# Kernel optimization log

Measured on AMD Instinct MI355X. Metric: run time of the kernel, lower is better.

Reference implementation:

```python
import jax, jax.numpy as jnp
import numpy as np

NUM_HEADS = 12
WIN = 7  # window_size[0] == window_size[1]


def setup_inputs() -> dict:
    key = jax.random.key(0)
    ks = jax.random.split(key, 8)
    B_, N, C = 2048, WIN * WIN, 384
    nW = 64
    return {
        "x": jax.random.normal(ks[0], (B_, N, C), dtype=jnp.float32),
        "mask": jax.random.normal(ks[1], (nW, N, N), dtype=jnp.float32),
        "qkv_w": jax.random.normal(ks[2], (3 * C, C), dtype=jnp.float32) * 0.02,
        "qkv_b": jax.random.normal(ks[3], (3 * C,), dtype=jnp.float32) * 0.02,
        "proj_w": jax.random.normal(ks[4], (C, C), dtype=jnp.float32) * 0.02,
        "proj_b": jax.random.normal(ks[5], (C,), dtype=jnp.float32) * 0.02,
        "rpb_table": jax.random.normal(ks[6], ((2 * WIN - 1) ** 2, NUM_HEADS), dtype=jnp.float32) * 0.02,
        "rel_index": jax.random.randint(ks[7], (N * N,), 0, (2 * WIN - 1) ** 2, dtype=jnp.int32),
    }


def reference(x, mask, qkv_w, qkv_b, proj_w, proj_b, rpb_table, rel_index):
    B_, N, C = x.shape
    H = NUM_HEADS
    d = C // H
    scale = d ** -0.5

    # QKV projection (quant wrappers act as identity in non-quant state)
    qkv = x @ qkv_w.T + qkv_b                      # [B_, N, 3C]
    qkv = qkv.reshape(B_, N, 3, H, d).transpose(2, 0, 3, 1, 4)  # [3, B_, H, N, d]
    q, k, v = qkv[0], qkv[1], qkv[2]

    attn = jnp.einsum("bhnd,bhmd->bhnm", q * scale, k)  # [B_, H, N, N]

    # relative position bias gather: [N*N] -> [N, N, H] -> [H, N, N]
    bias = rpb_table[rel_index].reshape(N, N, H).transpose(2, 0, 1)
    attn = attn + bias[None]

    # shifted-window mask add
    nW = mask.shape[0]
    attn = attn.reshape(B_ // nW, nW, H, N, N) + mask[None, :, None]
    attn = attn.reshape(B_, H, N, N)

    attn = jax.nn.softmax(attn, axis=-1)

    out = jnp.einsum("bhnm,bhmd->bhnd", attn, v)   # [B_, H, N, d]
    out = out.transpose(0, 2, 1, 3).reshape(B_, N, C)
    out = out @ proj_w.T + proj_b
    return out, attn
```

## Files before the change

kernel.cpp:

```cpp
#include <hip/hip_runtime.h>
#include <hip/hip_bf16.h>
#include <stdint.h>

#define H_ 12
#define D_ 32
#define N_ 49
#define C_ 384
#define B_TOT 2048
#define BH 24576
#define M_ROWS 100352
#define SCALE 0.17677669529663689f

typedef float f32x4 __attribute__((ext_vector_type(4)));
typedef __bf16 bf16x8 __attribute__((ext_vector_type(8)));
typedef unsigned short ushortx8 __attribute__((ext_vector_type(8)));

static __device__ __forceinline__ unsigned short f2bf(float f) {
  __bf16 b = (__bf16)f;
  return __builtin_bit_cast(unsigned short, b);
}

#define GL16(gp, lp)                                                        \
  __builtin_amdgcn_global_load_lds(                                         \
      (const __attribute__((address_space(1))) unsigned int*)(gp),          \
      (__attribute__((address_space(3))) unsigned int*)(lp), 16, 0, 0)

__global__ void prep(const float* __restrict__ x, const float* __restrict__ wq,
                     const float* __restrict__ wpw, const float* __restrict__ mask,
                     const float* __restrict__ rpb, const int* __restrict__ ridx,
                     unsigned short* __restrict__ x_bf,
                     unsigned short* __restrict__ wq_bf,
                     unsigned short* __restrict__ wp_bf,
                     float* __restrict__ comb) {
  const int blk = blockIdx.x, tid = threadIdx.x;
  if (blk < 2048) {
    for (int i = blk * 256 + tid; i < 4816896; i += 2048 * 256) {
      float4 a = ((const float4*)x)[2 * i];
      float4 b = ((const float4*)x)[2 * i + 1];
      ushortx8 v;
      v[0] = f2bf(a.x); v[1] = f2bf(a.y); v[2] = f2bf(a.z); v[3] = f2bf(a.w);
      v[4] = f2bf(b.x); v[5] = f2bf(b.y); v[6] = f2bf(b.z); v[7] = f2bf(b.w);
      *(ushortx8*)&x_bf[(size_t)i * 8] = v;
    }
  } else if (blk < 2264) {
    const int i = (blk - 2048) * 256 + tid;
    float4 a = ((const float4*)wq)[2 * i];
    float4 b = ((const float4*)wq)[2 * i + 1];
    ushortx8 v;
    v[0] = f2bf(a.x); v[1] = f2bf(a.y); v[2] = f2bf(a.z); v[3] = f2bf(a.w);
    v[4] = f2bf(b.x); v[5] = f2bf(b.y); v[6] = f2bf(b.z); v[7] = f2bf(b.w);
    *(ushortx8*)&wq_bf[(size_t)i * 8] = v;
  } else if (blk < 2336) {
    const int i = (blk - 2264) * 256 + tid;
    float4 a = ((const float4*)wpw)[2 * i];
    float4 b = ((const float4*)wpw)[2 * i + 1];
    ushortx8 v;
    v[0] = f2bf(a.x); v[1] = f2bf(a.y); v[2] = f2bf(a.z); v[3] = f2bf(a.w);
    v[4] = f2bf(b.x); v[5] = f2bf(b.y); v[6] = f2bf(b.z); v[7] = f2bf(b.w);
    *(ushortx8*)&wp_bf[(size_t)i * 8] = v;
  } else {
    const int wh = blk - 2336;
    const int w = wh / 12, h = wh - w * 12;
    float* cb = comb + (size_t)wh * 4096;
    const float* mw = mask + (size_t)w * N_ * N_;
    for (int e = tid; e < 4096; e += 256) {
      const int r = e >> 6, c = e & 63;
      float v;
      if (c >= N_) v = -1e30f;
      else if (r >= N_) v = 0.0f;
      else v = mw[r * N_ + c] + rpb[ridx[r * N_ + c] * H_ + h];
      cb[e] = v;
    }
  }
}

__global__ __launch_bounds__(256, 4)
void qkv_gemm(const unsigned short* __restrict__ A,
              const unsigned short* __restrict__ W,
              const float* __restrict__ bias, unsigned short* __restrict__ qkv) {
  __shared__ __align__(16) unsigned short smem[16384];
  const int tid = threadIdx.x;
  const int w = blockIdx.x;
  const int t = (w & 7) * 882 + (w >> 3);
  const int bm = t / 9, bn = t - bm * 9;
  const int lane = tid & 63, wv = tid >> 6;
  const int wm = wv >> 1, wn = wv & 1;
  const int lo = lane & 15, hi = lane >> 4;

  const int sr0 = tid >> 2, sq0 = (tid & 3) ^ ((sr0 >> 1) & 3);
  const int ci1 = tid + 256;
  const int sr1 = ci1 >> 2, sq1 = (ci1 & 3) ^ ((sr1 >> 1) & 3);

  const unsigned short* Ab = A + (size_t)bm * 128 * 384;
  const unsigned short* Wb = W + (size_t)bn * 128 * 384;

  f32x4 acc[4][4];
#pragma unroll
  for (int i = 0; i < 4; i++)
#pragma unroll
    for (int j = 0; j < 4; j++)
#pragma unroll
      for (int r = 0; r < 4; r++) acc[i][j][r] = 0.0f;

  {
    unsigned short* b0 = smem;
    GL16(Ab + sr0 * 384 + sq0 * 8, b0 + tid * 8);
    GL16(Ab + sr1 * 384 + sq1 * 8, b0 + ci1 * 8);
    GL16(Wb + sr0 * 384 + sq0 * 8, b0 + 4096 + tid * 8);
    GL16(Wb + sr1 * 384 + sq1 * 8, b0 + 4096 + ci1 * 8);
  }
  __syncthreads();

  int buf = 0;
  for (int kt = 0; kt < 12; kt++) {
    if (kt < 11) {
      const int kk = (kt + 1) * 32;
      unsigned short* nb = smem + (buf ^ 1) * 8192;
      GL16(Ab + sr0 * 384 + kk + sq0 * 8, nb + tid * 8);
      GL16(Ab + sr1 * 384 + kk + sq1 * 8, nb + ci1 * 8);
      GL16(Wb + sr0 * 384 + kk + sq0 * 8, nb + 4096 + tid * 8);
      GL16(Wb + sr1 * 384 + kk + sq1 * 8, nb + 4096 + ci1 * 8);
    }
    const unsigned short* ba = smem + buf * 8192;
    bf16x8 af[4], bfm[4];
#pragma unroll
    for (int mt = 0; mt < 4; mt++) {
      const int row = wm * 64 + mt * 16 + lo;
      af[mt] = *(const bf16x8*)&ba[(row * 4 + (hi ^ ((row >> 1) & 3))) * 8];
    }
#pragma unroll
    for (int nt = 0; nt < 4; nt++) {
      const int row = wn * 64 + nt * 16 + lo;
      bfm[nt] = *(const bf16x8*)&ba[4096 + (row * 4 + (hi ^ ((row >> 1) & 3))) * 8];
    }
#pragma unroll
    for (int mt = 0; mt < 4; mt++)
#pragma unroll
      for (int nt = 0; nt < 4; nt++)
        acc[mt][nt] = __builtin_amdgcn_mfma_f32_16x16x32_bf16(af[mt], bfm[nt], acc[mt][nt], 0, 0, 0);
    __syncthreads();
    buf ^= 1;
  }

  unsigned short* ep = smem + wv * 4096;
#pragma unroll
  for (int nt = 0; nt < 4; nt++) {
    const int j = bn * 128 + wn * 64 + nt * 16 + lo;
    const float bj = bias[j];
    const float mul = (j < 384) ? SCALE : 1.0f;
    const int c16 = nt * 2 + (lo >> 3);
    const int wi = lo & 7;
#pragma unroll
    for (int mt = 0; mt < 4; mt++) {
#pragma unroll
      for (int r = 0; r < 4; r++) {
        const int row = mt * 16 + hi * 4 + r;
        ep[row * 64 + ((c16 ^ hi) << 3) + wi] = f2bf((acc[mt][nt][r] + bj) * mul);
      }
    }
  }
#pragma unroll
  for (int cc = 0; cc < 2; cc++) {
    const int cidx = cc * 64 + lane;
    const int lr = cidx >> 1, lch = cidx & 1;
    const int i = bm * 128 + wm * 64 + lr;
    const int b = i / 49, sq = i - b * 49;
    const int j0 = bn * 128 + wn * 64 + lch * 32;
    const int which = j0 / 384;
    const int rem = j0 - which * 384;
    const int h = rem >> 5;
    const int hlr = (lr >> 2) & 3;
    unsigned short* dst = qkv + ((size_t)which * BH + (size_t)b * H_ + h) * (N_ * D_) + sq * D_;
#pragma unroll
    for (int q = 0; q < 4; q++) {
      const int c16r = lch * 4 + q;
      *(uint4*)(dst + q * 8) = *(const uint4*)&ep[lr * 64 + ((c16r ^ hlr) << 3)];
    }
  }
}

__global__ __launch_bounds__(64, 2)
void attn_kernel(const unsigned short* __restrict__ qkv,
                 const float* __restrict__ comb,
                 float* __restrict__ probs,
                 unsigned short* __restrict__ av) {
  __shared__ __align__(16) unsigned short P[64 * 72];
  __shared__ __align__(16) unsigned short VT[32 * 72];
  const int lane = threadIdx.x;
  const int lo = lane & 15, hi = lane >> 4;
  const int h = blockIdx.x, b = blockIdx.y;

  const unsigned short* qp = qkv + (size_t)(b * H_ + h) * (N_ * D_);
  const unsigned short* kp = qp + (size_t)BH * (N_ * D_);
  const unsigned short* vp = kp + (size_t)BH * (N_ * D_);

  {
    unsigned int* vz = (unsigned int*)VT;
#pragma unroll
    for (int i = 0; i < 18; i++) vz[lane + 64 * i] = 0u;
  }
  __syncthreads();

  bf16x8 aq[4], bk[4];
#pragma unroll
  for (int t = 0; t < 4; t++) {
    aq[t] = *(const bf16x8*)(qp + (t * 16 + lo) * D_ + hi * 8);
    bk[t] = *(const bf16x8*)(kp + (t * 16 + lo) * D_ + hi * 8);
  }
  f32x4 s[4][4];
#pragma unroll
  for (int mt = 0; mt < 4; mt++)
#pragma unroll
    for (int nt = 0; nt < 4; nt++) {
#pragma unroll
      for (int r = 0; r < 4; r++) s[mt][nt][r] = 0.0f;
      s[mt][nt] = __builtin_amdgcn_mfma_f32_16x16x32_bf16(aq[mt], bk[nt], s[mt][nt], 0, 0, 0);
    }

#pragma unroll
  for (int it = 0; it < 4; it++) {
    const int idx = it * 64 + lane;
    if (idx < 196) {
      const int sq = idx >> 2, ch = idx & 3;
      ushortx8 vv = *(const ushortx8*)(vp + sq * D_ + ch * 8);
#pragma unroll
      for (int jj = 0; jj < 8; jj++) VT[(ch * 8 + jj) * 72 + sq] = vv[jj];
    }
  }

  const float* cb = comb + (size_t)((b & 63) * H_ + h) * 4096;
#pragma unroll
  for (int mt = 0; mt < 4; mt++) {
#pragma unroll
    for (int r = 0; r < 4; r++) {
      const int row = mt * 16 + hi * 4 + r;
      const float* crow = cb + row * 64 + lo;
      float v0 = s[mt][0][r] + crow[0];
      float v1 = s[mt][1][r] + crow[16];
      float v2 = s[mt][2][r] + crow[32];
      float v3 = s[mt][3][r] + crow[48];
      float m = fmaxf(fmaxf(v0, v1), fmaxf(v2, v3));
      m = fmaxf(m, __shfl_xor(m, 1));
      m = fmaxf(m, __shfl_xor(m, 2));
      m = fmaxf(m, __shfl_xor(m, 4));
      m = fmaxf(m, __shfl_xor(m, 8));
      v0 = __expf(v0 - m); v1 = __expf(v1 - m);
      v2 = __expf(v2 - m); v3 = __expf(v3 - m);
      float sum = v0 + v1 + v2 + v3;
      sum += __shfl_xor(sum, 1);
      sum += __shfl_xor(sum, 2);
      sum += __shfl_xor(sum, 4);
      sum += __shfl_xor(sum, 8);
      const float rinv = 1.0f / sum;
      s[mt][0][r] = v0 * rinv; s[mt][1][r] = v1 * rinv;
      s[mt][2][r] = v2 * rinv; s[mt][3][r] = v3 * rinv;
    }
  }

  const size_t pbase = (size_t)(b * H_ + h) * N_ * N_;
#pragma unroll
  for (int mt = 0; mt < 4; mt++) {
#pragma unroll
    for (int r = 0; r < 4; r++) {
      const int row = mt * 16 + hi * 4 + r;
      if (row < N_) {
#pragma unroll
        for (int nt = 0; nt < 4; nt++) {
          const int c = nt * 16 + lo;
          if (c < N_) probs[pbase + row * N_ + c] = s[mt][nt][r];
        }
      }
#pragma unroll
      for (int nt = 0; nt < 4; nt++)
        P[row * 72 + nt * 16 + lo] = f2bf(s[mt][nt][r]);
    }
  }
  __syncthreads();

  f32x4 o[4][2];
#pragma unroll
  for (int mt = 0; mt < 4; mt++)
#pragma unroll
    for (int n2 = 0; n2 < 2; n2++)
#pragma unroll
      for (int r = 0; r < 4; r++) o[mt][n2][r] = 0.0f;
#pragma unroll
  for (int ks = 0; ks < 2; ks++) {
    bf16x8 pa[4], vb[2];
#pragma unroll
    for (int mt = 0; mt < 4; mt++)
      pa[mt] = *(const bf16x8*)&P[(mt * 16 + lo) * 72 + ks * 32 + hi * 8];
#pragma unroll
    for (int n2 = 0; n2 < 2; n2++)
      vb[n2] = *(const bf16x8*)&VT[(n2 * 16 + lo) * 72 + ks * 32 + hi * 8];
#pragma unroll
    for (int mt = 0; mt < 4; mt++)
#pragma unroll
      for (int n2 = 0; n2 < 2; n2++)
        o[mt][n2] = __builtin_amdgcn_mfma_f32_16x16x32_bf16(pa[mt], vb[n2], o[mt][n2], 0, 0, 0);
  }

  __syncthreads();
#pragma unroll
  for (int mt = 0; mt < 4; mt++) {
#pragma unroll
    for (int r = 0; r < 4; r++) {
      const int row = mt * 16 + hi * 4 + r;
      if (row < N_) {
#pragma unroll
        for (int n2 = 0; n2 < 2; n2++)
          P[row * 40 + n2 * 16 + lo] = f2bf(o[mt][n2][r]);
      }
    }
  }
  if (lane < N_) {
    unsigned short* dst = av + ((size_t)b * N_ + lane) * C_ + h * D_;
    const unsigned short* src = P + lane * 40;
#pragma unroll
    for (int q = 0; q < 4; q++)
      *(uint4*)(dst + q * 8) = *(const uint4*)(src + q * 8);
  }
}

__global__ __launch_bounds__(256, 4)
void proj_gemm(const unsigned short* __restrict__ A,
               const unsigned short* __restrict__ W,
               const float* __restrict__ bias, float* __restrict__ out) {
  __shared__ __align__(16) unsigned short smem[16384];
  const int tid = threadIdx.x;
  const int w = blockIdx.x;
  const int t = (w & 7) * 294 + (w >> 3);
  const int bm = t / 3, bn = t - bm * 3;
  const int lane = tid & 63, wv = tid >> 6;
  const int wm = wv >> 1, wn = wv & 1;
  const int lo = lane & 15, hi = lane >> 4;

  const int sr0 = tid >> 2, sq0 = (tid & 3) ^ ((sr0 >> 1) & 3);
  const int ci1 = tid + 256;
  const int sr1 = ci1 >> 2, sq1 = (ci1 & 3) ^ ((sr1 >> 1) & 3);

  const unsigned short* Ab = A + (size_t)bm * 128 * 384;
  const unsigned short* Wb = W + (size_t)bn * 128 * 384;

  f32x4 acc[4][4];
#pragma unroll
  for (int i = 0; i < 4; i++)
#pragma unroll
    for (int j = 0; j < 4; j++)
#pragma unroll
      for (int r = 0; r < 4; r++) acc[i][j][r] = 0.0f;

  {
    unsigned short* b0 = smem;
    GL16(Ab + sr0 * 384 + sq0 * 8, b0 + tid * 8);
    GL16(Ab + sr1 * 384 + sq1 * 8, b0 + ci1 * 8);
    GL16(Wb + sr0 * 384 + sq0 * 8, b0 + 4096 + tid * 8);
    GL16(Wb + sr1 * 384 + sq1 * 8, b0 + 4096 + ci1 * 8);
  }
  __syncthreads();

  int buf = 0;
  for (int kt = 0; kt < 12; kt++) {
    if (kt < 11) {
      const int kk = (kt + 1) * 32;
      unsigned short* nb = smem + (buf ^ 1) * 8192;
      GL16(Ab + sr0 * 384 + kk + sq0 * 8, nb + tid * 8);
      GL16(Ab + sr1 * 384 + kk + sq1 * 8, nb + ci1 * 8);
      GL16(Wb + sr0 * 384 + kk + sq0 * 8, nb + 4096 + tid * 8);
      GL16(Wb + sr1 * 384 + kk + sq1 * 8, nb + 4096 + ci1 * 8);
    }
    const unsigned short* ba = smem + buf * 8192;
    bf16x8 af[4], bfm[4];
#pragma unroll
    for (int mt = 0; mt < 4; mt++) {
      const int row = wm * 64 + mt * 16 + lo;
      af[mt] = *(const bf16x8*)&ba[(row * 4 + (hi ^ ((row >> 1) & 3))) * 8];
    }
#pragma unroll
    for (int nt = 0; nt < 4; nt++) {
      const int row = wn * 64 + nt * 16 + lo;
      bfm[nt] = *(const bf16x8*)&ba[4096 + (row * 4 + (hi ^ ((row >> 1) & 3))) * 8];
    }
#pragma unroll
    for (int mt = 0; mt < 4; mt++)
#pragma unroll
      for (int nt = 0; nt < 4; nt++)
        acc[mt][nt] = __builtin_amdgcn_mfma_f32_16x16x32_bf16(af[mt], bfm[nt], acc[mt][nt], 0, 0, 0);
    __syncthreads();
    buf ^= 1;
  }

#pragma unroll
  for (int nt = 0; nt < 4; nt++) {
    const int j = bn * 128 + wn * 64 + nt * 16 + lo;
    const float bj = bias[j];
#pragma unroll
    for (int mt = 0; mt < 4; mt++) {
#pragma unroll
      for (int r = 0; r < 4; r++) {
        const int i = bm * 128 + wm * 64 + mt * 16 + hi * 4 + r;
        out[(size_t)i * 384 + j] = acc[mt][nt][r] + bj;
      }
    }
  }
}

extern "C" void kernel_launch(void* const* d_in, const int* in_sizes, int n_in,
                              void* d_out, int out_size, void* d_ws, size_t ws_size,
                              hipStream_t stream) {
  const float* x      = (const float*)d_in[0];
  const float* mask   = (const float*)d_in[1];
  const float* qkv_w  = (const float*)d_in[2];
  const float* qkv_b  = (const float*)d_in[3];
  const float* proj_w = (const float*)d_in[4];
  const float* proj_b = (const float*)d_in[5];
  const float* rpb    = (const float*)d_in[6];
  const int*   ridx   = (const int*)d_in[7];

  unsigned short* qkv   = (unsigned short*)d_ws;
  unsigned short* x_bf  = qkv + (size_t)3 * BH * N_ * D_;
  unsigned short* av    = x_bf;
  float* comb           = (float*)(x_bf + (size_t)M_ROWS * C_);
  unsigned short* wq_bf = (unsigned short*)(comb + 768 * 4096);
  unsigned short* wp_bf = wq_bf + 1152 * 384;
  float* out   = (float*)d_out;
  float* probs = out + (size_t)M_ROWS * C_;

  prep<<<3104, 256, 0, stream>>>(x, qkv_w, proj_w, mask, rpb, ridx,
                                 x_bf, wq_bf, wp_bf, comb);
  qkv_gemm<<<7056, 256, 0, stream>>>(x_bf, wq_bf, qkv_b, qkv);
  attn_kernel<<<dim3(H_, B_TOT), 64, 0, stream>>>(qkv, comb, probs, av);
  proj_gemm<<<2352, 256, 0, stream>>>(av, wp_bf, proj_b, out);
}
```

Before: 459.4 us.

## Fuse fp32-to-bf16 conversion of x into QKV GEMM loads and swizzle attention LDS

The QKV GEMM now reads fp32 activations directly through registers, converts them to bf16 and writes them into swizzled shared memory, so the separate conversion pass over x and its bf16 buffer disappear from prep. Each A tile is now read 9 times in fp32 across the N-blocks instead of in bf16, which doubles A-side global traffic in the GEMM, and occupancy is lowered to 3 blocks per CU to make room for the extra registers. Separately, the attention kernel's P and V^T shared buffers drop their padding in favour of an XOR swizzle to avoid bank conflicts.

```diff
diff --git a/kernel.cpp b/kernel.cpp
--- a/kernel.cpp
+++ b/kernel.cpp
@@ -20,46 +20,37 @@
   return __builtin_bit_cast(unsigned short, b);
 }
 
+static __device__ __forceinline__ uint4 pack8(float4 a, float4 b) {
+  ushortx8 v;
+  v[0] = f2bf(a.x); v[1] = f2bf(a.y); v[2] = f2bf(a.z); v[3] = f2bf(a.w);
+  v[4] = f2bf(b.x); v[5] = f2bf(b.y); v[6] = f2bf(b.z); v[7] = f2bf(b.w);
+  return __builtin_bit_cast(uint4, v);
+}
+
 #define GL16(gp, lp)                                                        \
   __builtin_amdgcn_global_load_lds(                                         \
       (const __attribute__((address_space(1))) unsigned int*)(gp),          \
       (__attribute__((address_space(3))) unsigned int*)(lp), 16, 0, 0)
 
-__global__ void prep(const float* __restrict__ x, const float* __restrict__ wq,
-                     const float* __restrict__ wpw, const float* __restrict__ mask,
-                     const float* __restrict__ rpb, const int* __restrict__ ridx,
-                     unsigned short* __restrict__ x_bf,
+__global__ void prep(const float* __restrict__ wq, const float* __restrict__ wpw,
+                     const float* __restrict__ mask, const float* __restrict__ rpb,
+                     const int* __restrict__ ridx,
                      unsigned short* __restrict__ wq_bf,
                      unsigned short* __restrict__ wp_bf,
                      float* __restrict__ comb) {
   const int blk = blockIdx.x, tid = threadIdx.x;
-  if (blk < 2048) {
-    for (int i = blk * 256 + tid; i < 4816896; i += 2048 * 256) {
-      float4 a = ((const float4*)x)[2 * i];
-      float4 b = ((const float4*)x)[2 * i + 1];
-      ushortx8 v;
-      v[0] = f2bf(a.x); v[1] = f2bf(a.y); v[2] = f2bf(a.z); v[3] = f2bf(a.w);
-      v[4] = f2bf(b.x); v[5] = f2bf(b.y); v[6] = f2bf(b.z); v[7] = f2bf(b.w);
-      *(ushortx8*)&x_bf[(size_t)i * 8] = v;
-    }
-  } else if (blk < 2264) {
-    const int i = (blk - 2048) * 256 + tid;
+  if (blk < 216) {
+    const int i = blk * 256 + tid;
     float4 a = ((const float4*)wq)[2 * i];
     float4 b = ((const float4*)wq)[2 * i + 1];
-    ushortx8 v;
-    v[0] = f2bf(a.x); v[1] = f2bf(a.y); v[2] = f2bf(a.z); v[3] = f2bf(a.w);
-    v[4] = f2bf(b.x); v[5] = f2bf(b.y); v[6] = f2bf(b.z); v[7] = f2bf(b.w);
-    *(ushortx8*)&wq_bf[(size_t)i * 8] = v;
-  } else if (blk < 2336) {
-    const int i = (blk - 2264) * 256 + tid;
+    *(uint4*)&wq_bf[(size_t)i * 8] = pack8(a, b);
+  } else if (blk < 288) {
+    const int i = (blk - 216) * 256 + tid;
     float4 a = ((const float4*)wpw)[2 * i];
     float4 b = ((const float4*)wpw)[2 * i + 1];
-    ushortx8 v;
-    v[0] = f2bf(a.x); v[1] = f2bf(a.y); v[2] = f2bf(a.z); v[3] = f2bf(a.w);
-    v[4] = f2bf(b.x); v[5] = f2bf(b.y); v[6] = f2bf(b.z); v[7] = f2bf(b.w);
-    *(ushortx8*)&wp_bf[(size_t)i * 8] = v;
+    *(uint4*)&wp_bf[(size_t)i * 8] = pack8(a, b);
   } else {
-    const int wh = blk - 2336;
+    const int wh = blk - 288;
     const int w = wh / 12, h = wh - w * 12;
     float* cb = comb + (size_t)wh * 4096;
     const float* mw = mask + (size_t)w * N_ * N_;
@@ -74,8 +65,8 @@
   }
 }
 
-__global__ __launch_bounds__(256, 4)
-void qkv_gemm(const unsigned short* __restrict__ A,
+__global__ __launch_bounds__(256, 3)
+void qkv_gemm(const float* __restrict__ A,
               const unsigned short* __restrict__ W,
               const float* __restrict__ bias, unsigned short* __restrict__ qkv) {
   __shared__ __align__(16) unsigned short smem[16384];
@@ -87,11 +78,14 @@
   const int wm = wv >> 1, wn = wv & 1;
   const int lo = lane & 15, hi = lane >> 4;
 
+  const int arow = tid >> 1, acg = tid & 1;
+  const int ac0 = (acg * 2) ^ ((arow >> 1) & 3);
+  const int ac1 = (acg * 2 + 1) ^ ((arow >> 1) & 3);
   const int sr0 = tid >> 2, sq0 = (tid & 3) ^ ((sr0 >> 1) & 3);
   const int ci1 = tid + 256;
   const int sr1 = ci1 >> 2, sq1 = (ci1 & 3) ^ ((sr1 >> 1) & 3);
 
-  const unsigned short* Ab = A + (size_t)bm * 128 * 384;
+  const float* Ab = A + (size_t)bm * 128 * 384 + arow * 384 + acg * 16;
   const unsigned short* Wb = W + (size_t)bn * 128 * 384;
 
   f32x4 acc[4][4];
@@ -103,21 +97,27 @@
       for (int r = 0; r < 4; r++) acc[i][j][r] = 0.0f;
 
   {
-    unsigned short* b0 = smem;
-    GL16(Ab + sr0 * 384 + sq0 * 8, b0 + tid * 8);
-    GL16(Ab + sr1 * 384 + sq1 * 8, b0 + ci1 * 8);
-    GL16(Wb + sr0 * 384 + sq0 * 8, b0 + 4096 + tid * 8);
-    GL16(Wb + sr1 * 384 + sq1 * 8, b0 + 4096 + ci1 * 8);
+    float4 s0 = *(const float4*)(Ab + 0);
+    float4 s1 = *(const float4*)(Ab + 4);
+    float4 s2 = *(const float4*)(Ab + 8);
+    float4 s3 = *(const float4*)(Ab + 12);
+    GL16(Wb + sr0 * 384 + sq0 * 8, smem + 4096 + tid * 8);
+    GL16(Wb + sr1 * 384 + sq1 * 8, smem + 4096 + ci1 * 8);
+    *(uint4*)&smem[(arow * 4 + ac0) * 8] = pack8(s0, s1);
+    *(uint4*)&smem[(arow * 4 + ac1) * 8] = pack8(s2, s3);
   }
   __syncthreads();
 
   int buf = 0;
   for (int kt = 0; kt < 12; kt++) {
+    float4 s0, s1, s2, s3;
     if (kt < 11) {
       const int kk = (kt + 1) * 32;
+      s0 = *(const float4*)(Ab + kk + 0);
+      s1 = *(const float4*)(Ab + kk + 4);
+      s2 = *(const float4*)(Ab + kk + 8);
+      s3 = *(const float4*)(Ab + kk + 12);
       unsigned short* nb = smem + (buf ^ 1) * 8192;
-      GL16(Ab + sr0 * 384 + kk + sq0 * 8, nb + tid * 8);
-      GL16(Ab + sr1 * 384 + kk + sq1 * 8, nb + ci1 * 8);
       GL16(Wb + sr0 * 384 + kk + sq0 * 8, nb + 4096 + tid * 8);
       GL16(Wb + sr1 * 384 + kk + sq1 * 8, nb + 4096 + ci1 * 8);
     }
@@ -138,6 +138,11 @@
 #pragma unroll
       for (int nt = 0; nt < 4; nt++)
         acc[mt][nt] = __builtin_amdgcn_mfma_f32_16x16x32_bf16(af[mt], bfm[nt], acc[mt][nt], 0, 0, 0);
+    if (kt < 11) {
+      unsigned short* nb = smem + (buf ^ 1) * 8192;
+      *(uint4*)&nb[(arow * 4 + ac0) * 8] = pack8(s0, s1);
+      *(uint4*)&nb[(arow * 4 + ac1) * 8] = pack8(s2, s3);
+    }
     __syncthreads();
     buf ^= 1;
   }
@@ -184,10 +189,11 @@
                  const float* __restrict__ comb,
                  float* __restrict__ probs,
                  unsigned short* __restrict__ av) {
-  __shared__ __align__(16) unsigned short P[64 * 72];
-  __shared__ __align__(16) unsigned short VT[32 * 72];
+  __shared__ __align__(16) unsigned short P[64 * 64];
+  __shared__ __align__(16) unsigned short VT[32 * 64];
   const int lane = threadIdx.x;
   const int lo = lane & 15, hi = lane >> 4;
+  const int l7 = lo & 7;
   const int h = blockIdx.x, b = blockIdx.y;
 
   const unsigned short* qp = qkv + (size_t)(b * H_ + h) * (N_ * D_);
@@ -197,7 +203,7 @@
   {
     unsigned int* vz = (unsigned int*)VT;
 #pragma unroll
-    for (int i = 0; i < 18; i++) vz[lane + 64 * i] = 0u;
+    for (int i = 0; i < 16; i++) vz[lane + 64 * i] = 0u;
   }
   __syncthreads();
 
@@ -224,7 +230,8 @@
       const int sq = idx >> 2, ch = idx & 3;
       ushortx8 vv = *(const ushortx8*)(vp + sq * D_ + ch * 8);
 #pragma unroll
-      for (int jj = 0; jj < 8; jj++) VT[(ch * 8 + jj) * 72 + sq] = vv[jj];
+      for (int jj = 0; jj < 8; jj++)
+        VT[(ch * 8 + jj) * 64 + (((sq >> 3) ^ jj) << 3) + (sq & 7)] = vv[jj];
     }
   }
 
@@ -270,9 +277,10 @@
           if (c < N_) probs[pbase + row * N_ + c] = s[mt][nt][r];
         }
       }
+      const int r7 = row & 7;
 #pragma unroll
       for (int nt = 0; nt < 4; nt++)
-        P[row * 72 + nt * 16 + lo] = f2bf(s[mt][nt][r]);
+        P[row * 64 + (((nt * 2 + (lo >> 3)) ^ r7) << 3) + l7] = f2bf(s[mt][nt][r]);
     }
   }
   __syncthreads();
@@ -289,10 +297,10 @@
     bf16x8 pa[4], vb[2];
 #pragma unroll
     for (int mt = 0; mt < 4; mt++)
-      pa[mt] = *(const bf16x8*)&P[(mt * 16 + lo) * 72 + ks * 32 + hi * 8];
+      pa[mt] = *(const bf16x8*)&P[(mt * 16 + lo) * 64 + (((ks * 4 + hi) ^ l7) << 3)];
 #pragma unroll
     for (int n2 = 0; n2 < 2; n2++)
-      vb[n2] = *(const bf16x8*)&VT[(n2 * 16 + lo) * 72 + ks * 32 + hi * 8];
+      vb[n2] = *(const bf16x8*)&VT[(n2 * 16 + lo) * 64 + (((ks * 4 + hi) ^ l7) << 3)];
 #pragma unroll
     for (int mt = 0; mt < 4; mt++)
 #pragma unroll
@@ -418,17 +426,16 @@
   const int*   ridx   = (const int*)d_in[7];
 
   unsigned short* qkv   = (unsigned short*)d_ws;
-  unsigned short* x_bf  = qkv + (size_t)3 * BH * N_ * D_;
-  unsigned short* av    = x_bf;
-  float* comb           = (float*)(x_bf + (size_t)M_ROWS * C_);
+  unsigned short* av    = qkv + (size_t)3 * BH * N_ * D_;
+  float* comb           = (float*)(av + (size_t)M_ROWS * C_);
   unsigned short* wq_bf = (unsigned short*)(comb + 768 * 4096);
   unsigned short* wp_bf = wq_bf + 1152 * 384;
   float* out   = (float*)d_out;
   float* probs = out + (size_t)M_ROWS * C_;
 
-  prep<<<3104, 256, 0, stream>>>(x, qkv_w, proj_w, mask, rpb, ridx,
-                                 x_bf, wq_bf, wp_bf, comb);
-  qkv_gemm<<<7056, 256, 0, stream>>>(x_bf, wq_bf, qkv_b, qkv);
+  prep<<<1056, 256, 0, stream>>>(qkv_w, proj_w, mask, rpb, ridx,
+                                 wq_bf, wp_bf, comb);
+  qkv_gemm<<<7056, 256, 0, stream>>>(x, wq_bf, qkv_b, qkv);
   attn_kernel<<<dim3(H_, B_TOT), 64, 0, stream>>>(qkv, comb, probs, av);
   proj_gemm<<<2352, 256, 0, stream>>>(av, wp_bf, proj_b, out);
 }
```

Result: slower. 511.8 us (+11.4%).

## Enlarge QKV GEMM tile to 256x128 and swizzle attention LDS buffers

Applied to the files above, without the earlier changes.

The QKV projection GEMM moves from 128x128 tiles with 4 waves to 256x128 tiles with 8 waves (512 threads). Each weight tile is loaded once per 256 activation rows, which halves weight traffic per output and halves the number of blocks. The attention kernel replaces padded LDS rows (stride 72) for P and the transposed V with unpadded 64-wide rows and an XOR chunk swizzle, to avoid bank conflicts and use less LDS. The cost is a larger per-block LDS footprint in the GEMM, which may lower how many blocks fit on each CU. The bf16 packing code is also folded into a helper.

```diff
diff --git a/kernel.cpp b/kernel.cpp
--- a/kernel.cpp
+++ b/kernel.cpp
@@ -18,6 +18,13 @@
 static __device__ __forceinline__ unsigned short f2bf(float f) {
   __bf16 b = (__bf16)f;
   return __builtin_bit_cast(unsigned short, b);
+}
+
+static __device__ __forceinline__ uint4 pack8(float4 a, float4 b) {
+  ushortx8 v;
+  v[0] = f2bf(a.x); v[1] = f2bf(a.y); v[2] = f2bf(a.z); v[3] = f2bf(a.w);
+  v[4] = f2bf(b.x); v[5] = f2bf(b.y); v[6] = f2bf(b.z); v[7] = f2bf(b.w);
+  return __builtin_bit_cast(uint4, v);
 }
 
 #define GL16(gp, lp)                                                        \
@@ -37,27 +44,18 @@
     for (int i = blk * 256 + tid; i < 4816896; i += 2048 * 256) {
       float4 a = ((const float4*)x)[2 * i];
       float4 b = ((const float4*)x)[2 * i + 1];
-      ushortx8 v;
-      v[0] = f2bf(a.x); v[1] = f2bf(a.y); v[2] = f2bf(a.z); v[3] = f2bf(a.w);
-      v[4] = f2bf(b.x); v[5] = f2bf(b.y); v[6] = f2bf(b.z); v[7] = f2bf(b.w);
-      *(ushortx8*)&x_bf[(size_t)i * 8] = v;
+      *(uint4*)&x_bf[(size_t)i * 8] = pack8(a, b);
     }
   } else if (blk < 2264) {
     const int i = (blk - 2048) * 256 + tid;
     float4 a = ((const float4*)wq)[2 * i];
     float4 b = ((const float4*)wq)[2 * i + 1];
-    ushortx8 v;
-    v[0] = f2bf(a.x); v[1] = f2bf(a.y); v[2] = f2bf(a.z); v[3] = f2bf(a.w);
-    v[4] = f2bf(b.x); v[5] = f2bf(b.y); v[6] = f2bf(b.z); v[7] = f2bf(b.w);
-    *(ushortx8*)&wq_bf[(size_t)i * 8] = v;
+    *(uint4*)&wq_bf[(size_t)i * 8] = pack8(a, b);
   } else if (blk < 2336) {
     const int i = (blk - 2264) * 256 + tid;
     float4 a = ((const float4*)wpw)[2 * i];
     float4 b = ((const float4*)wpw)[2 * i + 1];
-    ushortx8 v;
-    v[0] = f2bf(a.x); v[1] = f2bf(a.y); v[2] = f2bf(a.z); v[3] = f2bf(a.w);
-    v[4] = f2bf(b.x); v[5] = f2bf(b.y); v[6] = f2bf(b.z); v[7] = f2bf(b.w);
-    *(ushortx8*)&wp_bf[(size_t)i * 8] = v;
+    *(uint4*)&wp_bf[(size_t)i * 8] = pack8(a, b);
   } else {
     const int wh = blk - 2336;
     const int w = wh / 12, h = wh - w * 12;
@@ -74,24 +72,24 @@
   }
 }
 
-__global__ __launch_bounds__(256, 4)
+__global__ __launch_bounds__(512, 4)
 void qkv_gemm(const unsigned short* __restrict__ A,
               const unsigned short* __restrict__ W,
               const float* __restrict__ bias, unsigned short* __restrict__ qkv) {
-  __shared__ __align__(16) unsigned short smem[16384];
+  __shared__ __align__(16) unsigned short smem[32768];
   const int tid = threadIdx.x;
   const int w = blockIdx.x;
-  const int t = (w & 7) * 882 + (w >> 3);
+  const int t = (w & 7) * 441 + (w >> 3);
   const int bm = t / 9, bn = t - bm * 9;
   const int lane = tid & 63, wv = tid >> 6;
   const int wm = wv >> 1, wn = wv & 1;
   const int lo = lane & 15, hi = lane >> 4;
 
-  const int sr0 = tid >> 2, sq0 = (tid & 3) ^ ((sr0 >> 1) & 3);
-  const int ci1 = tid + 256;
-  const int sr1 = ci1 >> 2, sq1 = (ci1 & 3) ^ ((sr1 >> 1) & 3);
-
-  const unsigned short* Ab = A + (size_t)bm * 128 * 384;
+  const int ar0 = tid >> 2,  aq0 = (tid & 3) ^ ((ar0 >> 1) & 3);
+  const int aci1 = tid + 512;
+  const int ar1 = aci1 >> 2, aq1 = (aci1 & 3) ^ ((ar1 >> 1) & 3);
+
+  const unsigned short* Ab = A + (size_t)bm * 256 * 384;
   const unsigned short* Wb = W + (size_t)bn * 128 * 384;
 
   f32x4 acc[4][4];
@@ -104,10 +102,9 @@
 
   {
     unsigned short* b0 = smem;
-    GL16(Ab + sr0 * 384 + sq0 * 8, b0 + tid * 8);
-    GL16(Ab + sr1 * 384 + sq1 * 8, b0 + ci1 * 8);
-    GL16(Wb + sr0 * 384 + sq0 * 8, b0 + 4096 + tid * 8);
-    GL16(Wb + sr1 * 384 + sq1 * 8, b0 + 4096 + ci1 * 8);
+    GL16(Ab + ar0 * 384 + aq0 * 8, b0 + tid * 8);
+    GL16(Ab + ar1 * 384 + aq1 * 8, b0 + aci1 * 8);
+    GL16(Wb + ar0 * 384 + aq0 * 8, b0 + 8192 + tid * 8);
   }
   __syncthreads();
 
@@ -115,13 +112,12 @@
   for (int kt = 0; kt < 12; kt++) {
     if (kt < 11) {
       const int kk = (kt + 1) * 32;
-      unsigned short* nb = smem + (buf ^ 1) * 8192;
-      GL16(Ab + sr0 * 384 + kk + sq0 * 8, nb + tid * 8);
-      GL16(Ab + sr1 * 384 + kk + sq1 * 8, nb + ci1 * 8);
-      GL16(Wb + sr0 * 384 + kk + sq0 * 8, nb + 4096 + tid * 8);
-      GL16(Wb + sr1 * 384 + kk + sq1 * 8, nb + 4096 + ci1 * 8);
-    }
-    const unsigned short* ba = smem + buf * 8192;
+      unsigned short* nb = smem + (buf ^ 1) * 12288;
+      GL16(Ab + ar0 * 384 + kk + aq0 * 8, nb + tid * 8);
+      GL16(Ab + ar1 * 384 + kk + aq1 * 8, nb + aci1 * 8);
+      GL16(Wb + ar0 * 384 + kk + aq0 * 8, nb + 8192 + tid * 8);
+    }
+    const unsigned short* ba = smem + buf * 12288;
     bf16x8 af[4], bfm[4];
 #pragma unroll
     for (int mt = 0; mt < 4; mt++) {
@@ -131,7 +127,7 @@
 #pragma unroll
     for (int nt = 0; nt < 4; nt++) {
       const int row = wn * 64 + nt * 16 + lo;
-      bfm[nt] = *(const bf16x8*)&ba[4096 + (row * 4 + (hi ^ ((row >> 1) & 3))) * 8];
+      bfm[nt] = *(const bf16x8*)&ba[8192 + (row * 4 + (hi ^ ((row >> 1) & 3))) * 8];
     }
 #pragma unroll
     for (int mt = 0; mt < 4; mt++)
@@ -163,7 +159,7 @@
   for (int cc = 0; cc < 2; cc++) {
     const int cidx = cc * 64 + lane;
     const int lr = cidx >> 1, lch = cidx & 1;
-    const int i = bm * 128 + wm * 64 + lr;
+    const int i = bm * 256 + wm * 64 + lr;
     const int b = i / 49, sq = i - b * 49;
     const int j0 = bn * 128 + wn * 64 + lch * 32;
     const int which = j0 / 384;
@@ -184,10 +180,11 @@
                  const float* __restrict__ comb,
                  float* __restrict__ probs,
                  unsigned short* __restrict__ av) {
-  __shared__ __align__(16) unsigned short P[64 * 72];
-  __shared__ __align__(16) unsigned short VT[32 * 72];
+  __shared__ __align__(16) unsigned short P[64 * 64];
+  __shared__ __align__(16) unsigned short VT[32 * 64];
   const int lane = threadIdx.x;
   const int lo = lane & 15, hi = lane >> 4;
+  const int l7 = lo & 7;
   const int h = blockIdx.x, b = blockIdx.y;
 
   const unsigned short* qp = qkv + (size_t)(b * H_ + h) * (N_ * D_);
@@ -197,7 +194,7 @@
   {
     unsigned int* vz = (unsigned int*)VT;
 #pragma unroll
-    for (int i = 0; i < 18; i++) vz[lane + 64 * i] = 0u;
+    for (int i = 0; i < 16; i++) vz[lane + 64 * i] = 0u;
   }
   __syncthreads();
 
@@ -224,7 +221,8 @@
       const int sq = idx >> 2, ch = idx & 3;
       ushortx8 vv = *(const ushortx8*)(vp + sq * D_ + ch * 8);
 #pragma unroll
-      for (int jj = 0; jj < 8; jj++) VT[(ch * 8 + jj) * 72 + sq] = vv[jj];
+      for (int jj = 0; jj < 8; jj++)
+        VT[(ch * 8 + jj) * 64 + (((sq >> 3) ^ jj) << 3) + (sq & 7)] = vv[jj];
     }
   }
 
@@ -270,9 +268,10 @@
           if (c < N_) probs[pbase + row * N_ + c] = s[mt][nt][r];
         }
       }
+      const int r7 = row & 7;
 #pragma unroll
       for (int nt = 0; nt < 4; nt++)
-        P[row * 72 + nt * 16 + lo] = f2bf(s[mt][nt][r]);
+        P[row * 64 + (((nt * 2 + (lo >> 3)) ^ r7) << 3) + l7] = f2bf(s[mt][nt][r]);
     }
   }
   __syncthreads();
@@ -289,10 +288,10 @@
     bf16x8 pa[4], vb[2];
 #pragma unroll
     for (int mt = 0; mt < 4; mt++)
-      pa[mt] = *(const bf16x8*)&P[(mt * 16 + lo) * 72 + ks * 32 + hi * 8];
+      pa[mt] = *(const bf16x8*)&P[(mt * 16 + lo) * 64 + (((ks * 4 + hi) ^ l7) << 3)];
 #pragma unroll
     for (int n2 = 0; n2 < 2; n2++)
-      vb[n2] = *(const bf16x8*)&VT[(n2 * 16 + lo) * 72 + ks * 32 + hi * 8];
+      vb[n2] = *(const bf16x8*)&VT[(n2 * 16 + lo) * 64 + (((ks * 4 + hi) ^ l7) << 3)];
 #pragma unroll
     for (int mt = 0; mt < 4; mt++)
 #pragma unroll
@@ -428,7 +427,7 @@
 
   prep<<<3104, 256, 0, stream>>>(x, qkv_w, proj_w, mask, rpb, ridx,
                                  x_bf, wq_bf, wp_bf, comb);
-  qkv_gemm<<<7056, 256, 0, stream>>>(x_bf, wq_bf, qkv_b, qkv);
+  qkv_gemm<<<3528, 512, 0, stream>>>(x_bf, wq_bf, qkv_b, qkv);
   attn_kernel<<<dim3(H_, B_TOT), 64, 0, stream>>>(qkv, comb, probs, av);
   proj_gemm<<<2352, 256, 0, stream>>>(av, wp_bf, proj_b, out);
 }
```

Measured after the change: 466.5 us. Within noise of the previous version (+1.5%).
